# Kernel optimization log

Hardware: AMD Instinct MI355X
Metric: run time of the kernel (lower is better)

Reference implementation:

```python
import jax, jax.numpy as jnp
import numpy as np

_DN = ('NCHW', 'OIHW', 'NCHW')


def _gaussian_kernel1d(ksize, sigma):
    x = np.arange(ksize, dtype=np.float32) - ksize // 2
    g = np.exp(-x ** 2 / (2.0 * sigma ** 2))
    return (g / g.sum()).astype(np.float32)


def _nms_kernels():
    # kornia get_canny_nms_kernel: kernel k = center - neighbor at angle k*45deg (0deg = +x/right)
    k = np.zeros((8, 1, 3, 3), dtype=np.float32)
    offs = [(0, 1), (-1, 1), (-1, 0), (-1, -1), (0, -1), (1, -1), (1, 0), (1, 1)]
    for i, (dy, dx) in enumerate(offs):
        k[i, 0, 1, 1] = 1.0
        k[i, 0, 1 + dy, 1 + dx] = -1.0
    return k


def _conv(x, w, padding):
    return jax.lax.conv_general_dilated(x, w, (1, 1), padding, dimension_numbers=_DN)


def _canny_magnitude(data):
    eps = 1e-6
    x = (data + 1.0) / 2.0
    # rgb -> grayscale (kornia weights)
    rgb_w = jnp.array([0.299, 0.587, 0.114], dtype=x.dtype)
    gray = jnp.einsum('bchw,c->bhw', x, rgb_w)[:, None]  # [B,1,H,W]
    # gaussian blur 5x5, sigma=1, reflect border (kornia default), separable
    g1d = jnp.asarray(_gaussian_kernel1d(5, 1.0), dtype=x.dtype)
    p = jnp.pad(gray, ((0, 0), (0, 0), (2, 2), (2, 2)), mode='reflect')
    blurred = _conv(_conv(p, g1d.reshape(1, 1, 1, 5), 'VALID'), g1d.reshape(1, 1, 5, 1), 'VALID')
    # sobel spatial gradient (normalized=False), replicate padding
    sob_x = jnp.array([[-1., 0., 1.], [-2., 0., 2.], [-1., 0., 1.]], dtype=x.dtype)
    sob = jnp.stack([sob_x, sob_x.T])[:, None]  # [2,1,3,3]
    bp = jnp.pad(blurred, ((0, 0), (0, 0), (1, 1), (1, 1)), mode='edge')
    grads = _conv(bp, sob, 'VALID')  # [B,2,H,W]
    gx, gy = grads[:, 0:1], grads[:, 1:2]
    magnitude = jnp.sqrt(gx * gx + gy * gy + eps)  # [B,1,H,W]
    # angle rounded to nearest 45 degrees
    ang45 = jnp.round(jnp.rad2deg(jnp.arctan2(gy, gx)) / 45.0)
    # non-maximum suppression: center-minus-neighbor along 8 directions (zero pad)
    nms_k = jnp.asarray(_nms_kernels(), dtype=x.dtype)
    nms_mag = _conv(magnitude, nms_k, ((1, 1), (1, 1)))  # [B,8,H,W]
    idx_pos = ang45.astype(jnp.int32) % 8
    idx_neg = (idx_pos + 4) % 8
    sel_pos = jnp.take_along_axis(nms_mag, idx_pos, axis=1)
    sel_neg = jnp.take_along_axis(nms_mag, idx_neg, axis=1)
    is_max = jnp.minimum(sel_pos, sel_neg) > 0.0
    return magnitude * is_max


def setup_inputs() -> dict:
    key = jax.random.key(0)
    data = jax.random.normal(key, (16, 3, 512, 512), dtype=jnp.float32)
    return {'data': data}


def reference(data):
    # EdgeOperator.forward: canny((data+1)/2)[0] -> NMS'd gradient magnitude [B,1,H,W]
    return _canny_magnitude(data)
```

## Files before the change

### kernel.cpp

```cpp
#include <hip/hip_runtime.h>
#include <math.h>

#define IMH 512
#define IMW 512
#define RB    16
#define NBAND 32
#define NWC   10
#define OUTW  56

__device__ __forceinline__ int reflect_i(int v, int n) {
    if (v < 0) v = -v;
    if (v >= n) v = 2 * n - 2 - v;
    return v;
}
__device__ __forceinline__ float dpp_shr1(float x) {
    int i = __float_as_int(x);
    return __int_as_float(__builtin_amdgcn_update_dpp(i, i, 0x138, 0xF, 0xF, false));
}
__device__ __forceinline__ float dpp_shl1(float x) {
    int i = __float_as_int(x);
    return __int_as_float(__builtin_amdgcn_update_dpp(i, i, 0x130, 0xF, 0xF, false));
}

template <bool YB, bool XB>
__device__ __forceinline__ void run_band(const float* __restrict__ p0,
                                         const float* __restrict__ p1,
                                         const float* __restrict__ p2,
                                         float* __restrict__ outp,
                                         int y0, int c0, int lane) {
    const float w0 = 0.05448868f, w1 = 0.24420134f, w2 = 0.40261995f;
    const int cx = c0 + lane;
    const int rx = XB ? reflect_i(cx, IMW) : cx;
    int ixm = lane - 1, ixp = lane + 1;
    if (XB) {
        ixm = (cx - 1 < 0 ? 0 : (cx - 1 >= IMW ? IMW - 1 : cx - 1)) - c0;
        ixp = (cx + 1 < 0 ? 0 : (cx + 1 >= IMW ? IMW - 1 : cx + 1)) - c0;
    }
    const bool storeok = (lane >= 4) && (lane < 60) &&
                         (!XB || (unsigned)cx < (unsigned)IMW);

    float h0 = 0, h1 = 0, h2 = 0, h3 = 0;
    float b_1 = 0, b_0 = 0, bl_1 = 0, bl_0 = 0, br_1 = 0, br_0 = 0;
    float m_1 = 0, m_0 = 0, ml_1 = 0, ml_0 = 0, mr_1 = 0, mr_0 = 0;
    float gxp = 0, gyp = 0;

    float rr[4], gg[4], bb[4];
    #pragma unroll
    for (int k = 0; k < 4; ++k) {
        int y = y0 - 4 + k;
        int yo = (YB ? reflect_i(y, IMH) : y) * IMW + rx;
        rr[k] = p0[yo]; gg[k] = p1[yo]; bb[k] = p2[yo];
    }

    #pragma unroll
    for (int k = 0; k < RB + 8; ++k) {
        const int yL = y0 - 4 + k;
        const int sl = k & 3;
        float gray = 0.1495f * rr[sl] + 0.2935f * gg[sl] + 0.057f * bb[sl];
        if (k + 4 < RB + 8) {
            int y = yL + 4;
            int yo = (YB ? reflect_i(y, IMH) : y) * IMW + rx;
            rr[sl] = p0[yo]; gg[sl] = p1[yo]; bb[sl] = p2[yo];
        }
        float gm1 = dpp_shr1(gray);
        float gm2 = dpp_shr1(gm1);
        float gp1 = dpp_shl1(gray);
        float gp2 = dpp_shl1(gp1);
        float hnew = w0 * (gm2 + gp2) + w1 * (gm1 + gp1) + w2 * gray;

        float bnew = 0, blnew = 0, brnew = 0;
        if (k >= 4) {
            bnew = w0 * (h0 + hnew) + w1 * (h1 + h3) + w2 * h2;
            if (XB) { blnew = __shfl(bnew, ixm); brnew = __shfl(bnew, ixp); }
            else    { blnew = dpp_shr1(bnew);    brnew = dpp_shl1(bnew); }
        }

        float mnew = 0, mlnew = 0, mrnew = 0, gx = 0, gy = 0;
        if (k >= 6) {
            int u = yL - 3;
            float ta = b_1, tla = bl_1, tra = br_1;
            float tb = bnew, tlb = blnew, trb = brnew;
            if (YB) {
                if (u == 0)       { ta = b_0; tla = bl_0; tra = br_0; }
                if (u == IMH - 1) { tb = b_0; tlb = bl_0; trb = br_0; }
            }
            gx = (tra - tla) + 2.0f * (br_0 - bl_0) + (trb - tlb);
            gy = (tlb - tla) + 2.0f * (tb - ta) + (trb - tra);
            mnew = __builtin_amdgcn_sqrtf(gx * gx + gy * gy + 1e-6f);
            if (XB) { if ((unsigned)cx >= (unsigned)IMW) mnew = 0.0f; }
            mlnew = dpp_shr1(mnew);
            mrnew = dpp_shl1(mnew);
        }

        if (k >= 8) {
            int s = yL - 4;
            float pm = m_1, pml = ml_1, pmr = mr_1;
            float nm = mnew, nml = mlnew, nmr = mrnew;
            if (YB) {
                if (s == 0)       { pm = 0; pml = 0; pmr = 0; }
                if (s == IMH - 1) { nm = 0; nml = 0; nmr = 0; }
            }
            float ax = fabsf(gxp), ay = fabsf(gyp);
            bool ew = (ay <= 0.41421356237f * ax);
            bool ns = (ay >= 2.41421356237f * ax);
            bool d1 = (gxp * gyp > 0.0f);
            float n1 = ew ? mr_0 : (ns ? nm : (d1 ? pmr : nmr));
            float n2 = ew ? ml_0 : (ns ? pm : (d1 ? nml : pml));
            float mag = m_0;
            float o = (mag > n1 && mag > n2) ? mag : 0.0f;
            if (storeok)
                __builtin_nontemporal_store(o, &outp[(size_t)s * IMW + cx]);
        }

        h0 = h1; h1 = h2; h2 = h3; h3 = hnew;
        b_1 = b_0;  b_0 = bnew;
        bl_1 = bl_0; bl_0 = blnew;
        br_1 = br_0; br_0 = brnew;
        m_1 = m_0;  m_0 = mnew;
        ml_1 = ml_0; ml_0 = mlnew;
        mr_1 = mr_0; mr_0 = mrnew;
        gxp = gx; gyp = gy;
    }
}

__global__ __launch_bounds__(256, 4)
void canny_stream(const float* __restrict__ data, float* __restrict__ out) {
    const int lane = threadIdx.x & 63;
    const int xcd = blockIdx.x & 7;
    const int seq = blockIdx.x >> 3;
    const int lw  = (seq << 2) | (threadIdx.x >> 6);
    const int wc   = lw % NWC;
    const int t    = lw / NWC;
    const int band = t & (NBAND - 1);
    const int bat  = (xcd << 1) | (t >> 5);

    const int c0 = OUTW * wc - 4;
    const int y0 = band * RB;

    const size_t plane = (size_t)(IMH * IMW);
    const float* p0 = data + (size_t)bat * 3 * plane;
    const float* p1 = p0 + plane;
    const float* p2 = p1 + plane;
    float* outp = out + (size_t)bat * plane;

    const bool yb = (band == 0) || (band == NBAND - 1);
    const bool xb = (wc == 0) || (wc == NWC - 1);
    if (yb) {
        if (xb) run_band<true, true >(p0, p1, p2, outp, y0, c0, lane);
        else    run_band<true, false>(p0, p1, p2, outp, y0, c0, lane);
    } else {
        if (xb) run_band<false, true >(p0, p1, p2, outp, y0, c0, lane);
        else    run_band<false, false>(p0, p1, p2, outp, y0, c0, lane);
    }
}

extern "C" void kernel_launch(void* const* d_in, const int* in_sizes, int n_in,
                              void* d_out, int out_size, void* d_ws, size_t ws_size,
                              hipStream_t stream) {
    const float* data = (const float*)d_in[0];
    float* out = (float*)d_out;
    int B = in_sizes[0] / (3 * IMH * IMW);
    int blocks = (B * NBAND * NWC) / 4;
    canny_stream<<<blocks, dim3(256, 1, 1), 0, stream>>>(data, out);
}
```

Measured before the change: 88.91 us.

## Process four columns per lane with vector loads and wide column strips

Each lane now handles four adjacent columns using float4 loads and stores, so a wavefront covers about 248 output columns instead of 56. This cuts the halo recomputation and the redundant overlapping loads across column tiles, with a scalar strip covering the right edge. It also drops the XCD-aware block mapping and the templated boundary specialisations, so reflect and clamp checks now run on every band, and it lowers launch bounds to 2 blocks per CU because of the higher register use. Far fewer wavefronts exist (3 per band), which reduces parallelism and may hurt latency hiding.

```diff
diff --git a/kernel.cpp b/kernel.cpp
--- a/kernel.cpp
+++ b/kernel.cpp
@@ -5,14 +5,19 @@
 #define IMW 512
 #define RB    16
 #define NBAND 32
-#define NWC   10
-#define OUTW  56
+
+typedef __attribute__((ext_vector_type(4))) float f32x4;
 
 __device__ __forceinline__ int reflect_i(int v, int n) {
     if (v < 0) v = -v;
     if (v >= n) v = 2 * n - 2 - v;
     return v;
 }
+__device__ __forceinline__ int reflect_row(int y) {
+    int a = y < 0 ? -y : y;
+    int b = 2 * IMH - 2 - a;
+    return a < b ? a : b;
+}
 __device__ __forceinline__ float dpp_shr1(float x) {
     int i = __float_as_int(x);
     return __int_as_float(__builtin_amdgcn_update_dpp(i, i, 0x138, 0xF, 0xF, false));
@@ -22,22 +27,204 @@
     return __int_as_float(__builtin_amdgcn_update_dpp(i, i, 0x130, 0xF, 0xF, false));
 }
 
-template <bool YB, bool XB>
-__device__ __forceinline__ void run_band(const float* __restrict__ p0,
-                                         const float* __restrict__ p1,
-                                         const float* __restrict__ p2,
-                                         float* __restrict__ outp,
-                                         int y0, int c0, int lane) {
+
+struct V4S {
+    float rr[4][4], gg[4][4], bb[4][4];
+    float h0[4], h1[4], h2[4], h3[4];
+    float b1[4], b0[4], b1L, b1R, b0L, b0R;
+    float m1[4], m0[4], m1L, m1R, m0L, m0R;
+    float gxp[4], gyp[4];
+};
+
+__device__ __forceinline__ void vload(const float* __restrict__ p, int ro, int cx0,
+                                      bool a0, float r[4]) {
+    if (a0) {
+        r[0] = p[ro + 4]; r[1] = p[ro + 3]; r[2] = p[ro + 2]; r[3] = p[ro + 1];
+    } else {
+        f32x4 v = *reinterpret_cast<const f32x4*>(p + ro + cx0);
+        r[0] = v.x; r[1] = v.y; r[2] = v.z; r[3] = v.w;
+    }
+}
+
+template <int SL, bool DO_B, bool DO_M, bool DO_ST, bool REFILL>
+__device__ __forceinline__ void vstep(V4S& S, int yL,
+        const float* __restrict__ p0, const float* __restrict__ p1,
+        const float* __restrict__ p2, float* __restrict__ outp,
+        int cx0, bool a0, bool clampL, bool storeok) {
+    const float w0 = 0.05448868f, w1 = 0.24420134f, w2 = 0.40261995f;
+    float g[4];
+    #pragma unroll
+    for (int j = 0; j < 4; ++j)
+        g[j] = 0.1495f * S.rr[SL][j] + 0.2935f * S.gg[SL][j] + 0.057f * S.bb[SL][j];
+    if (REFILL) {
+        int ro = reflect_row(yL + 4) * IMW;
+        vload(p0, ro, cx0, a0, S.rr[SL]);
+        vload(p1, ro, cx0, a0, S.gg[SL]);
+        vload(p2, ro, cx0, a0, S.bb[SL]);
+    }
+    float Lm1 = dpp_shr1(g[3]), Lm2 = dpp_shr1(g[2]);
+    float Rp1 = dpp_shl1(g[0]), Rp2 = dpp_shl1(g[1]);
+    float hn[4];
+    hn[0] = w0 * (Lm2 + g[2]) + w1 * (Lm1 + g[1]) + w2 * g[0];
+    hn[1] = w0 * (Lm1 + g[3]) + w1 * (g[0] + g[2]) + w2 * g[1];
+    hn[2] = w0 * (g[0] + Rp1) + w1 * (g[1] + g[3]) + w2 * g[2];
+    hn[3] = w0 * (g[1] + Rp2) + w1 * (g[2] + Rp1) + w2 * g[3];
+
+    float bn[4] = {0, 0, 0, 0};
+    float bnL = 0, bnR = 0;
+    if (DO_B) {
+        #pragma unroll
+        for (int j = 0; j < 4; ++j)
+            bn[j] = w0 * (S.h0[j] + hn[j]) + w1 * (S.h1[j] + S.h3[j]) + w2 * S.h2[j];
+        bnL = dpp_shr1(bn[3]); bnR = dpp_shl1(bn[0]);
+    }
+    float mn[4] = {0, 0, 0, 0}, gx[4] = {0, 0, 0, 0}, gy[4] = {0, 0, 0, 0};
+    float mnL = 0, mnR = 0;
+    if (DO_M) {
+        const int u = yL - 3;
+        float ta[4], tb[4], taL, taR, tbL, tbR;
+        #pragma unroll
+        for (int j = 0; j < 4; ++j) { ta[j] = S.b1[j]; tb[j] = bn[j]; }
+        taL = S.b1L; taR = S.b1R; tbL = bnL; tbR = bnR;
+        if (u == 0) {
+            #pragma unroll
+            for (int j = 0; j < 4; ++j) ta[j] = S.b0[j];
+            taL = S.b0L; taR = S.b0R;
+        }
+        if (u == IMH - 1) {
+            #pragma unroll
+            for (int j = 0; j < 4; ++j) tb[j] = S.b0[j];
+            tbL = S.b0L; tbR = S.b0R;
+        }
+        if (clampL) { taL = ta[0]; tbL = tb[0]; }
+        const float b0Ledge = clampL ? S.b0[0] : S.b0L;
+        #pragma unroll
+        for (int j = 0; j < 4; ++j) {
+            float tla = (j == 0) ? taL : ta[j - 1];
+            float tra = (j == 3) ? taR : ta[j + 1];
+            float tlb = (j == 0) ? tbL : tb[j - 1];
+            float trb = (j == 3) ? tbR : tb[j + 1];
+            float bl0 = (j == 0) ? b0Ledge : S.b0[j - 1];
+            float br0 = (j == 3) ? S.b0R : S.b0[j + 1];
+            gx[j] = (tra - tla) + 2.0f * (br0 - bl0) + (trb - tlb);
+            gy[j] = (tlb - tla) + 2.0f * (tb[j] - ta[j]) + (trb - tra);
+            mn[j] = __builtin_amdgcn_sqrtf(gx[j] * gx[j] + gy[j] * gy[j] + 1e-6f);
+        }
+        if (a0) mn[3] = 0.0f;
+        mnL = dpp_shr1(mn[3]); mnR = dpp_shl1(mn[0]);
+    }
+    if (DO_ST) {
+        const int s = yL - 4;
+        float pm[4], nm[4], pmL, pmR, nmL, nmR;
+        #pragma unroll
+        for (int j = 0; j < 4; ++j) { pm[j] = S.m1[j]; nm[j] = mn[j]; }
+        pmL = S.m1L; pmR = S.m1R; nmL = mnL; nmR = mnR;
+        if (s == 0) {
+            #pragma unroll
+            for (int j = 0; j < 4; ++j) pm[j] = 0.0f;
+            pmL = 0.0f; pmR = 0.0f;
+        }
+        if (s == IMH - 1) {
+            #pragma unroll
+            for (int j = 0; j < 4; ++j) nm[j] = 0.0f;
+            nmL = 0.0f; nmR = 0.0f;
+        }
+        float o[4];
+        #pragma unroll
+        for (int j = 0; j < 4; ++j) {
+            float pml = (j == 0) ? pmL : pm[j - 1];
+            float pmr = (j == 3) ? pmR : pm[j + 1];
+            float nml = (j == 0) ? nmL : nm[j - 1];
+            float nmr = (j == 3) ? nmR : nm[j + 1];
+            float ml0 = (j == 0) ? S.m0L : S.m0[j - 1];
+            float mr0 = (j == 3) ? S.m0R : S.m0[j + 1];
+            float ax = fabsf(S.gxp[j]), ay = fabsf(S.gyp[j]);
+            bool ew = (ay <= 0.41421356237f * ax);
+            bool ns = (ay >= 2.41421356237f * ax);
+            bool d1 = (S.gxp[j] * S.gyp[j] > 0.0f);
+            float n1 = ew ? mr0 : (ns ? nm[j] : (d1 ? pmr : nmr));
+            float n2 = ew ? ml0 : (ns ? pm[j] : (d1 ? nml : pml));
+            float mag = S.m0[j];
+            o[j] = (mag > n1 && mag > n2) ? mag : 0.0f;
+        }
+        if (storeok) {
+            f32x4 v; v.x = o[0]; v.y = o[1]; v.z = o[2]; v.w = o[3];
+            __builtin_nontemporal_store(v,
+                reinterpret_cast<f32x4*>(outp + (size_t)s * IMW + cx0));
+        }
+    }
+    #pragma unroll
+    for (int j = 0; j < 4; ++j) {
+        S.h0[j] = S.h1[j]; S.h1[j] = S.h2[j]; S.h2[j] = S.h3[j]; S.h3[j] = hn[j];
+        S.b1[j] = S.b0[j]; S.b0[j] = bn[j];
+        S.m1[j] = S.m0[j]; S.m0[j] = mn[j];
+        S.gxp[j] = gx[j];  S.gyp[j] = gy[j];
+    }
+    S.b1L = S.b0L; S.b1R = S.b0R; S.b0L = bnL; S.b0R = bnR;
+    S.m1L = S.m0L; S.m1R = S.m0R; S.m0L = mnL; S.m0R = mnR;
+}
+
+__device__ __forceinline__ void run_band_v4(const float* __restrict__ p0,
+                                            const float* __restrict__ p1,
+                                            const float* __restrict__ p2,
+                                            float* __restrict__ outp,
+                                            int y0, int c0, int lane, bool isA) {
+    const int cx0 = c0 + 4 * lane;
+    const bool a0 = isA && (lane == 0);
+    const bool clampL = isA && (lane == 1);
+    const bool storeok = isA ? (lane >= 1 && lane <= 62) : (lane >= 1 && lane <= 61);
+    V4S S;
+    #pragma unroll
+    for (int j = 0; j < 4; ++j) {
+        S.h0[j] = S.h1[j] = S.h2[j] = S.h3[j] = 0.0f;
+        S.b1[j] = S.b0[j] = 0.0f; S.m1[j] = S.m0[j] = 0.0f;
+        S.gxp[j] = S.gyp[j] = 0.0f;
+    }
+    S.b1L = S.b1R = S.b0L = S.b0R = 0.0f;
+    S.m1L = S.m1R = S.m0L = S.m0R = 0.0f;
+    #pragma unroll
+    for (int k = 0; k < 4; ++k) {
+        int ro = reflect_row(y0 - 4 + k) * IMW;
+        vload(p0, ro, cx0, a0, S.rr[k]);
+        vload(p1, ro, cx0, a0, S.gg[k]);
+        vload(p2, ro, cx0, a0, S.bb[k]);
+    }
+    vstep<0, false, false, false, true>(S, y0 - 4, p0, p1, p2, outp, cx0, a0, clampL, storeok);
+    vstep<1, false, false, false, true>(S, y0 - 3, p0, p1, p2, outp, cx0, a0, clampL, storeok);
+    vstep<2, false, false, false, true>(S, y0 - 2, p0, p1, p2, outp, cx0, a0, clampL, storeok);
+    vstep<3, false, false, false, true>(S, y0 - 1, p0, p1, p2, outp, cx0, a0, clampL, storeok);
+    vstep<0, true,  false, false, true>(S, y0 + 0, p0, p1, p2, outp, cx0, a0, clampL, storeok);
+    vstep<1, true,  false, false, true>(S, y0 + 1, p0, p1, p2, outp, cx0, a0, clampL, storeok);
+    vstep<2, true,  true,  false, true>(S, y0 + 2, p0, p1, p2, outp, cx0, a0, clampL, storeok);
+    vstep<3, true,  true,  false, true>(S, y0 + 3, p0, p1, p2, outp, cx0, a0, clampL, storeok);
+    #pragma unroll 1
+    for (int kb = 8; kb < RB + 4; kb += 4) {
+        int yL = y0 - 4 + kb;
+        vstep<0, true, true, true, true>(S, yL + 0, p0, p1, p2, outp, cx0, a0, clampL, storeok);
+        vstep<1, true, true, true, true>(S, yL + 1, p0, p1, p2, outp, cx0, a0, clampL, storeok);
+        vstep<2, true, true, true, true>(S, yL + 2, p0, p1, p2, outp, cx0, a0, clampL, storeok);
+        vstep<3, true, true, true, true>(S, yL + 3, p0, p1, p2, outp, cx0, a0, clampL, storeok);
+    }
+    {
+        int yL = y0 + RB;
+        vstep<0, true, true, true, false>(S, yL + 0, p0, p1, p2, outp, cx0, a0, clampL, storeok);
+        vstep<1, true, true, true, false>(S, yL + 1, p0, p1, p2, outp, cx0, a0, clampL, storeok);
+        vstep<2, true, true, true, false>(S, yL + 2, p0, p1, p2, outp, cx0, a0, clampL, storeok);
+        vstep<3, true, true, true, false>(S, yL + 3, p0, p1, p2, outp, cx0, a0, clampL, storeok);
+    }
+}
+
+__device__ __forceinline__ void run_band_sc(const float* __restrict__ p0,
+                                            const float* __restrict__ p1,
+                                            const float* __restrict__ p2,
+                                            float* __restrict__ outp,
+                                            int y0, int c0, int lane) {
     const float w0 = 0.05448868f, w1 = 0.24420134f, w2 = 0.40261995f;
     const int cx = c0 + lane;
-    const int rx = XB ? reflect_i(cx, IMW) : cx;
-    int ixm = lane - 1, ixp = lane + 1;
-    if (XB) {
-        ixm = (cx - 1 < 0 ? 0 : (cx - 1 >= IMW ? IMW - 1 : cx - 1)) - c0;
-        ixp = (cx + 1 < 0 ? 0 : (cx + 1 >= IMW ? IMW - 1 : cx + 1)) - c0;
-    }
-    const bool storeok = (lane >= 4) && (lane < 60) &&
-                         (!XB || (unsigned)cx < (unsigned)IMW);
+    const int rx = reflect_i(cx, IMW);
+    const int ixm = ((cx - 1 < 0) ? 0 : (cx - 1 >= IMW ? IMW - 1 : cx - 1)) - c0;
+    const int ixp = ((cx + 1 < 0) ? 0 : (cx + 1 >= IMW ? IMW - 1 : cx + 1)) - c0;
+    const bool storeok = (lane >= 4) && (lane < 60) && ((unsigned)cx < (unsigned)IMW);
 
     float h0 = 0, h1 = 0, h2 = 0, h3 = 0;
     float b_1 = 0, b_0 = 0, bl_1 = 0, bl_0 = 0, br_1 = 0, br_0 = 0;
@@ -47,8 +234,7 @@
     float rr[4], gg[4], bb[4];
     #pragma unroll
     for (int k = 0; k < 4; ++k) {
-        int y = y0 - 4 + k;
-        int yo = (YB ? reflect_i(y, IMH) : y) * IMW + rx;
+        int yo = reflect_row(y0 - 4 + k) * IMW + rx;
         rr[k] = p0[yo]; gg[k] = p1[yo]; bb[k] = p2[yo];
     }
 
@@ -58,8 +244,7 @@
         const int sl = k & 3;
         float gray = 0.1495f * rr[sl] + 0.2935f * gg[sl] + 0.057f * bb[sl];
         if (k + 4 < RB + 8) {
-            int y = yL + 4;
-            int yo = (YB ? reflect_i(y, IMH) : y) * IMW + rx;
+            int yo = reflect_row(yL + 4) * IMW + rx;
             rr[sl] = p0[yo]; gg[sl] = p1[yo]; bb[sl] = p2[yo];
         }
         float gm1 = dpp_shr1(gray);
@@ -71,8 +256,7 @@
         float bnew = 0, blnew = 0, brnew = 0;
         if (k >= 4) {
             bnew = w0 * (h0 + hnew) + w1 * (h1 + h3) + w2 * h2;
-            if (XB) { blnew = __shfl(bnew, ixm); brnew = __shfl(bnew, ixp); }
-            else    { blnew = dpp_shr1(bnew);    brnew = dpp_shl1(bnew); }
+            blnew = __shfl(bnew, ixm); brnew = __shfl(bnew, ixp);
         }
 
         float mnew = 0, mlnew = 0, mrnew = 0, gx = 0, gy = 0;
@@ -80,14 +264,12 @@
             int u = yL - 3;
             float ta = b_1, tla = bl_1, tra = br_1;
             float tb = bnew, tlb = blnew, trb = brnew;
-            if (YB) {
-                if (u == 0)       { ta = b_0; tla = bl_0; tra = br_0; }
-                if (u == IMH - 1) { tb = b_0; tlb = bl_0; trb = br_0; }
-            }
+            if (u == 0)       { ta = b_0; tla = bl_0; tra = br_0; }
+            if (u == IMH - 1) { tb = b_0; tlb = bl_0; trb = br_0; }
             gx = (tra - tla) + 2.0f * (br_0 - bl_0) + (trb - tlb);
             gy = (tlb - tla) + 2.0f * (tb - ta) + (trb - tra);
             mnew = __builtin_amdgcn_sqrtf(gx * gx + gy * gy + 1e-6f);
-            if (XB) { if ((unsigned)cx >= (unsigned)IMW) mnew = 0.0f; }
+            if ((unsigned)cx >= (unsigned)IMW) mnew = 0.0f;
             mlnew = dpp_shr1(mnew);
             mrnew = dpp_shl1(mnew);
         }
@@ -96,10 +278,8 @@
             int s = yL - 4;
             float pm = m_1, pml = ml_1, pmr = mr_1;
             float nm = mnew, nml = mlnew, nmr = mrnew;
-            if (YB) {
-                if (s == 0)       { pm = 0; pml = 0; pmr = 0; }
-                if (s == IMH - 1) { nm = 0; nml = 0; nmr = 0; }
-            }
+            if (s == 0)       { pm = 0; pml = 0; pmr = 0; }
+            if (s == IMH - 1) { nm = 0; nml = 0; nmr = 0; }
             float ax = fabsf(gxp), ay = fabsf(gyp);
             bool ew = (ay <= 0.41421356237f * ax);
             bool ns = (ay >= 2.41421356237f * ax);
@@ -123,18 +303,14 @@
     }
 }
 
-__global__ __launch_bounds__(256, 4)
+__global__ __launch_bounds__(256, 2)
 void canny_stream(const float* __restrict__ data, float* __restrict__ out) {
     const int lane = threadIdx.x & 63;
-    const int xcd = blockIdx.x & 7;
-    const int seq = blockIdx.x >> 3;
-    const int lw  = (seq << 2) | (threadIdx.x >> 6);
-    const int wc   = lw % NWC;
-    const int t    = lw / NWC;
+    const int gw = blockIdx.x * 4 + (threadIdx.x >> 6);
+    const int strip = gw % 3;
+    const int t = gw / 3;
     const int band = t & (NBAND - 1);
-    const int bat  = (xcd << 1) | (t >> 5);
-
-    const int c0 = OUTW * wc - 4;
+    const int bat = t >> 5;
     const int y0 = band * RB;
 
     const size_t plane = (size_t)(IMH * IMW);
@@ -143,14 +319,12 @@
     const float* p2 = p1 + plane;
     float* outp = out + (size_t)bat * plane;
 
-    const bool yb = (band == 0) || (band == NBAND - 1);
-    const bool xb = (wc == 0) || (wc == NWC - 1);
-    if (yb) {
-        if (xb) run_band<true, true >(p0, p1, p2, outp, y0, c0, lane);
-        else    run_band<true, false>(p0, p1, p2, outp, y0, c0, lane);
+    if (strip == 2) {
+        run_band_sc(p0, p1, p2, outp, y0, 488, lane);
+    } else if (strip == 0) {
+        run_band_v4(p0, p1, p2, outp, y0, -4, lane, true);
     } else {
-        if (xb) run_band<false, true >(p0, p1, p2, outp, y0, c0, lane);
-        else    run_band<false, false>(p0, p1, p2, outp, y0, c0, lane);
+        run_band_v4(p0, p1, p2, outp, y0, 244, lane, false);
     }
 }
 
@@ -160,6 +334,6 @@
     const float* data = (const float*)d_in[0];
     float* out = (float*)d_out;
     int B = in_sizes[0] / (3 * IMH * IMW);
-    int blocks = (B * NBAND * NWC) / 4;
+    int blocks = (B * NBAND * 3) / 4;
     canny_stream<<<blocks, dim3(256, 1, 1), 0, stream>>>(data, out);
 }
```

Measured after the change: 115.3 us. 1.3x slower.
